# Performance work log

Measured on AMD Instinct MI355X. Metric: run time of the kernel, lower is better.

The kernel has to match this reference:

```python
import jax, jax.numpy as jnp
import numpy as np

B, T, F, U = 256, 2048, 64, 10  # batch, timesteps, features, lstm units


def setup_inputs() -> dict:
    key = jax.random.key(0)
    k1, k2, k3, k4 = jax.random.split(key, 4)
    return {
        "x": jax.random.normal(k1, (B, T, F), dtype=jnp.float32),
        "kernel": jax.random.normal(k2, (F, 4 * U), dtype=jnp.float32) * 0.1,
        "recurrent_kernel": jax.random.normal(k3, (U, 4 * U), dtype=jnp.float32) * 0.1,
        "bias": jnp.zeros((4 * U,), dtype=jnp.float32),
        "dense_w": jax.random.normal(k4, (U, 1), dtype=jnp.float32) * 0.1,
        "dense_b": jnp.zeros((1,), dtype=jnp.float32),
    }


def reference(x, kernel, recurrent_kernel, bias, dense_w, dense_b):
    units = recurrent_kernel.shape[0]
    batch = x.shape[0]
    # Precompute input contribution for all timesteps: [B, T, 4U]
    xz = jnp.einsum('btf,fg->btg', x, kernel) + bias

    def step(carry, z_t):
        h, c = carry
        z = z_t + h @ recurrent_kernel  # [B, 4U]
        i, f, g, o = jnp.split(z, 4, axis=-1)  # Keras gate order: i, f, c, o
        i = jax.nn.sigmoid(i)
        f = jax.nn.sigmoid(f)
        g = jax.nn.soft_sign(g)       # activation='softsign'
        o = jax.nn.sigmoid(o)
        c = f * c + i * g
        h = o * jax.nn.soft_sign(c)
        return (h, c), None

    h0 = jnp.zeros((batch, units), dtype=x.dtype)
    (h, _), _ = jax.lax.scan(step, (h0, h0), jnp.swapaxes(xz, 0, 1))
    logit = h @ dense_w + dense_b  # [B, 1]
    return jax.nn.sigmoid(logit)
```

## Files before the change

kernel.cpp:

```cpp
#include <hip/hip_runtime.h>

#define B_ 256
#define T_ 2048
#define F_ 64
#define U_ 10
#define G_ 40
#define CH 64
#define NCH (T_ / CH)

__device__ __forceinline__ float rcp_f(float x) { return __builtin_amdgcn_rcpf(x); }
__device__ __forceinline__ float rdlane_f(float v, int l) {
  return __int_as_float(__builtin_amdgcn_readlane(__float_as_int(v), l));
}
template <int CTRL>
__device__ __forceinline__ float qbcast(float v) {
  return __int_as_float(
      __builtin_amdgcn_update_dpp(0, __float_as_int(v), CTRL, 0xF, 0xF, true));
}

__global__ __launch_bounds__(256, 1) void lstm_fused(
    const float* __restrict__ x, const float* __restrict__ W,
    const float* __restrict__ R, const float* __restrict__ bias,
    const float* __restrict__ dw, const float* __restrict__ db,
    float* __restrict__ out) {
  __shared__ float zb[2][CH * G_];
  const int b = blockIdx.x;
  const int tid = threadIdx.x;
  const int wave = tid >> 6;
  const int lane = tid & 63;
  const float* xbase = x + (size_t)b * T_ * F_;

  if (wave == 0) {
    const int L = (lane < G_) ? lane : (G_ - 1);
    const int u = L >> 2, gate = L & 3;
    const int col = gate * U_ + u;
    float Rc[U_];
    #pragma unroll
    for (int j = 0; j < U_; ++j) Rc[j] = R[j * G_ + col];
    const float dwu = dw[u];
    const float db0 = db[0];
    float h = 0.f, c = 0.f;
    __syncthreads();
    for (int cc = 0; cc < NCH; ++cc) {
      const float* zrow = zb[cc & 1] + L;
      float zpf[4];
      #pragma unroll
      for (int k = 0; k < 4; ++k) zpf[k] = zrow[k * G_];
      for (int t0 = 0; t0 < CH; t0 += 4) {
        #pragma unroll
        for (int k = 0; k < 4; ++k) {
          float z0 = zpf[k];
          int tn = t0 + 4 + k;
          if (tn > CH - 1) tn = CH - 1;
          zpf[k] = zrow[tn * G_];
          float z1 = 0.f;
          #pragma unroll
          for (int j = 0; j < U_; j += 2) {
            float ha = rdlane_f(h, 4 * j);
            float hb = rdlane_f(h, 4 * (j + 1));
            z0 = fmaf(ha, Rc[j], z0);
            z1 = fmaf(hb, Rc[j + 1], z1);
          }
          float zz = z0 + z1;
          float sg = rcp_f(1.f + __expf(-zz));
          float ss = zz * rcp_f(1.f + __builtin_fabsf(zz));
          float a = (gate == 2) ? ss : sg;
          float ai = qbcast<0x00>(a);
          float af = qbcast<0x55>(a);
          float ag = qbcast<0xAA>(a);
          float ao = qbcast<0xFF>(a);
          c = fmaf(af, c, ai * ag);
          h = ao * c * rcp_f(1.f + __builtin_fabsf(c));
        }
      }
      __syncthreads();
    }
    float p = h * dwu;
    float logit = db0;
    #pragma unroll
    for (int j = 0; j < U_; ++j) logit += rdlane_f(p, 4 * j);
    if (lane == 0) out[b] = rcp_f(1.f + __expf(-logit));
  } else {
    const int p0 = tid - 64;
    const int p = (p0 < 160) ? p0 : 159;
    const bool act = (p0 < 160);
    const int s = p % G_;
    const int tsl = p / G_;
    const int u = s >> 2, gate = s & 3;
    const int col = gate * U_ + u;
    float wc[F_];
    #pragma unroll
    for (int k = 0; k < F_; ++k) wc[k] = W[k * G_ + col];
    const float bcol = bias[col];

    auto dot64 = [&](const float4* rb) {
      float z0 = bcol, z1 = 0.f, z2 = 0.f, z3 = 0.f;
      #pragma unroll
      for (int j = 0; j < 16; j += 4) {
        float4 a0 = rb[j], a1 = rb[j + 1], a2 = rb[j + 2], a3 = rb[j + 3];
        z0 = fmaf(a0.x, wc[4*j+0], z0);  z0 = fmaf(a0.y, wc[4*j+1], z0);
        z0 = fmaf(a0.z, wc[4*j+2], z0);  z0 = fmaf(a0.w, wc[4*j+3], z0);
        z1 = fmaf(a1.x, wc[4*j+4], z1);  z1 = fmaf(a1.y, wc[4*j+5], z1);
        z1 = fmaf(a1.z, wc[4*j+6], z1);  z1 = fmaf(a1.w, wc[4*j+7], z1);
        z2 = fmaf(a2.x, wc[4*j+8], z2);  z2 = fmaf(a2.y, wc[4*j+9], z2);
        z2 = fmaf(a2.z, wc[4*j+10], z2); z2 = fmaf(a2.w, wc[4*j+11], z2);
        z3 = fmaf(a3.x, wc[4*j+12], z3); z3 = fmaf(a3.y, wc[4*j+13], z3);
        z3 = fmaf(a3.z, wc[4*j+14], z3); z3 = fmaf(a3.w, wc[4*j+15], z3);
      }
      return (z0 + z1) + (z2 + z3);
    };

    auto produce = [&](int cc) {
      const float4* xr = (const float4*)(xbase + (size_t)cc * CH * F_);
      float* zrow = zb[cc & 1];
      float4 A[16], Bv[16];
      #pragma unroll
      for (int j = 0; j < 16; ++j) A[j] = xr[tsl * 16 + j];
      for (int it = 0; it < 16; it += 2) {
        const int t0 = tsl + 4 * it;
        const int t1 = t0 + 4;
        #pragma unroll
        for (int j = 0; j < 16; ++j) Bv[j] = xr[t1 * 16 + j];
        float za = dot64(A);
        if (act) zrow[t0 * G_ + s] = za;
        const int t2 = (it + 2 < 16) ? t0 + 8 : t0;
        #pragma unroll
        for (int j = 0; j < 16; ++j) A[j] = xr[t2 * 16 + j];
        float zbv = dot64(Bv);
        if (act) zrow[t1 * G_ + s] = zbv;
      }
    };

    produce(0);
    __syncthreads();
    for (int cc = 0; cc < NCH; ++cc) {
      if (cc + 1 < NCH) produce(cc + 1);
      __syncthreads();
    }
  }
}

extern "C" void kernel_launch(void* const* d_in, const int* in_sizes, int n_in,
                              void* d_out, int out_size, void* d_ws, size_t ws_size,
                              hipStream_t stream) {
  const float* x    = (const float*)d_in[0];
  const float* W    = (const float*)d_in[1];
  const float* R    = (const float*)d_in[2];
  const float* bias = (const float*)d_in[3];
  const float* dw   = (const float*)d_in[4];
  const float* db   = (const float*)d_in[5];
  float* out = (float*)d_out;
  (void)d_ws; (void)ws_size; (void)in_sizes; (void)n_in; (void)out_size;
  lstm_fused<<<B_, 256, 0, stream>>>(x, W, R, bias, dw, db, out);
}
```

Before: 408.2 us.

## Stage x chunks into LDS via direct global-to-LDS loads, raise recurrent wave priority

The producer waves no longer stream x from global memory into registers. They now issue global_load_lds DMA copies into a double-buffered LDS tile, two chunks ahead, and compute the input projection from LDS. The recurrent wave gets a higher scheduling priority through s_setprio, and both roles add one extra barrier so the prefetch and the barriers stay matched. The goal is to cut producer register pressure and its contention with the serial recurrence wave, at the cost of more LDS use and reliance on barrier-level wait counts for the async loads.

```diff
diff --git a/kernel.cpp b/kernel.cpp
--- a/kernel.cpp
+++ b/kernel.cpp
@@ -17,12 +17,18 @@
   return __int_as_float(
       __builtin_amdgcn_update_dpp(0, __float_as_int(v), CTRL, 0xF, 0xF, true));
 }
+__device__ __forceinline__ void gload_lds16(const float* g, float* l) {
+  __builtin_amdgcn_global_load_lds(
+      (const __attribute__((address_space(1))) void*)g,
+      (__attribute__((address_space(3))) void*)l, 16, 0, 0);
+}
 
 __global__ __launch_bounds__(256, 1) void lstm_fused(
     const float* __restrict__ x, const float* __restrict__ W,
     const float* __restrict__ R, const float* __restrict__ bias,
     const float* __restrict__ dw, const float* __restrict__ db,
     float* __restrict__ out) {
+  __shared__ float xb[2][CH * F_];
   __shared__ float zb[2][CH * G_];
   const int b = blockIdx.x;
   const int tid = threadIdx.x;
@@ -31,6 +37,7 @@
   const float* xbase = x + (size_t)b * T_ * F_;
 
   if (wave == 0) {
+    __builtin_amdgcn_s_setprio(3);
     const int L = (lane < G_) ? lane : (G_ - 1);
     const int u = L >> 2, gate = L & 3;
     const int col = gate * U_ + u;
@@ -40,6 +47,7 @@
     const float dwu = dw[u];
     const float db0 = db[0];
     float h = 0.f, c = 0.f;
+    __syncthreads();
     __syncthreads();
     for (int cc = 0; cc < NCH; ++cc) {
       const float* zrow = zb[cc & 1] + L;
@@ -70,7 +78,9 @@
           float ag = qbcast<0xAA>(a);
           float ao = qbcast<0xFF>(a);
           c = fmaf(af, c, ai * ag);
-          h = ao * c * rcp_f(1.f + __builtin_fabsf(c));
+          float oc = ao * c;
+          float den = 1.f + __builtin_fabsf(c);
+          h = oc * rcp_f(den);
         }
       }
       __syncthreads();
@@ -88,52 +98,47 @@
     const int tsl = p / G_;
     const int u = s >> 2, gate = s & 3;
     const int col = gate * U_ + u;
+    const int pw = wave - 1;
     float wc[F_];
     #pragma unroll
     for (int k = 0; k < F_; ++k) wc[k] = W[k * G_ + col];
     const float bcol = bias[col];
 
-    auto dot64 = [&](const float4* rb) {
-      float z0 = bcol, z1 = 0.f, z2 = 0.f, z3 = 0.f;
-      #pragma unroll
-      for (int j = 0; j < 16; j += 4) {
-        float4 a0 = rb[j], a1 = rb[j + 1], a2 = rb[j + 2], a3 = rb[j + 3];
-        z0 = fmaf(a0.x, wc[4*j+0], z0);  z0 = fmaf(a0.y, wc[4*j+1], z0);
-        z0 = fmaf(a0.z, wc[4*j+2], z0);  z0 = fmaf(a0.w, wc[4*j+3], z0);
-        z1 = fmaf(a1.x, wc[4*j+4], z1);  z1 = fmaf(a1.y, wc[4*j+5], z1);
-        z1 = fmaf(a1.z, wc[4*j+6], z1);  z1 = fmaf(a1.w, wc[4*j+7], z1);
-        z2 = fmaf(a2.x, wc[4*j+8], z2);  z2 = fmaf(a2.y, wc[4*j+9], z2);
-        z2 = fmaf(a2.z, wc[4*j+10], z2); z2 = fmaf(a2.w, wc[4*j+11], z2);
-        z3 = fmaf(a3.x, wc[4*j+12], z3); z3 = fmaf(a3.y, wc[4*j+13], z3);
-        z3 = fmaf(a3.z, wc[4*j+14], z3); z3 = fmaf(a3.w, wc[4*j+15], z3);
-      }
-      return (z0 + z1) + (z2 + z3);
+    auto load_x = [&](int cx) {
+      const float* g = xbase + (size_t)cx * CH * F_;
+      float* l = xb[cx & 1];
+      for (int i = pw; i < 16; i += 3)
+        gload_lds16(g + i * 256 + lane * 4, l + i * 256);
     };
-
-    auto produce = [&](int cc) {
-      const float4* xr = (const float4*)(xbase + (size_t)cc * CH * F_);
-      float* zrow = zb[cc & 1];
-      float4 A[16], Bv[16];
-      #pragma unroll
-      for (int j = 0; j < 16; ++j) A[j] = xr[tsl * 16 + j];
-      for (int it = 0; it < 16; it += 2) {
-        const int t0 = tsl + 4 * it;
-        const int t1 = t0 + 4;
+    auto produce = [&](int tc) {
+      const float* xr = xb[tc & 1];
+      float* zrow = zb[tc & 1];
+      for (int tt = tsl; tt < CH; tt += 4) {
+        const float4* row4 = (const float4*)(xr + tt * F_);
+        float z0 = bcol, z1 = 0.f, z2 = 0.f, z3 = 0.f;
         #pragma unroll
-        for (int j = 0; j < 16; ++j) Bv[j] = xr[t1 * 16 + j];
-        float za = dot64(A);
-        if (act) zrow[t0 * G_ + s] = za;
-        const int t2 = (it + 2 < 16) ? t0 + 8 : t0;
-        #pragma unroll
-        for (int j = 0; j < 16; ++j) A[j] = xr[t2 * 16 + j];
-        float zbv = dot64(Bv);
-        if (act) zrow[t1 * G_ + s] = zbv;
+        for (int j = 0; j < 16; j += 4) {
+          float4 a0 = row4[j], a1 = row4[j + 1], a2 = row4[j + 2], a3 = row4[j + 3];
+          z0 = fmaf(a0.x, wc[4*j+0], z0);  z0 = fmaf(a0.y, wc[4*j+1], z0);
+          z0 = fmaf(a0.z, wc[4*j+2], z0);  z0 = fmaf(a0.w, wc[4*j+3], z0);
+          z1 = fmaf(a1.x, wc[4*j+4], z1);  z1 = fmaf(a1.y, wc[4*j+5], z1);
+          z1 = fmaf(a1.z, wc[4*j+6], z1);  z1 = fmaf(a1.w, wc[4*j+7], z1);
+          z2 = fmaf(a2.x, wc[4*j+8], z2);  z2 = fmaf(a2.y, wc[4*j+9], z2);
+          z2 = fmaf(a2.z, wc[4*j+10], z2); z2 = fmaf(a2.w, wc[4*j+11], z2);
+          z3 = fmaf(a3.x, wc[4*j+12], z3); z3 = fmaf(a3.y, wc[4*j+13], z3);
+          z3 = fmaf(a3.z, wc[4*j+14], z3); z3 = fmaf(a3.w, wc[4*j+15], z3);
+        }
+        if (act) zrow[tt * G_ + s] = (z0 + z1) + (z2 + z3);
       }
     };
 
+    load_x(0);
+    load_x(1);
+    __syncthreads();
     produce(0);
     __syncthreads();
     for (int cc = 0; cc < NCH; ++cc) {
+      if (cc + 2 < NCH) load_x(cc + 2);
       if (cc + 1 < NCH) produce(cc + 1);
       __syncthreads();
     }
```

New measurement: 354.1 us. 1.15x faster.
